# Kernel optimization log

Hardware: AMD Instinct MI355X
Metric: run time of the kernel (lower is better)

The kernel has to match this reference:

```python
import jax, jax.numpy as jnp
import numpy as np

B, S, D, H, DK, FF, NQ = 4, 1024, 512, 64, 8, 2048, 8


def _layernorm(x, w, b, eps=1e-5):
    m = x.mean(-1, keepdims=True)
    v = ((x - m) ** 2).mean(-1, keepdims=True)
    return (x - m) / jnp.sqrt(v + eps) * w + b


def setup_inputs() -> dict:
    key = jax.random.key(0)
    ks = jax.random.split(key, 24)
    std = 0.02
    inp = {
        "x": jax.random.normal(ks[0], (B, S, D), dtype=jnp.float32),
        "Wq": jax.random.normal(ks[1], (D, D)) * std,
        "bq": jnp.zeros((D,)),
        "Wk": jax.random.normal(ks[2], (D, D)) * std,
        "bk": jnp.zeros((D,)),
        "Wv": jax.random.normal(ks[3], (D, D)) * std,
        "bv": jnp.zeros((D,)),
        "theta_attn": jax.random.normal(ks[4], (DK,)) * 0.1,  # trainable RX angles
        "gate_attn": jnp.asarray(1.0, dtype=jnp.float32),
        "Wo": jax.random.normal(ks[5], (D, D)) * std,
        "bo": jnp.zeros((D,)),
        "ln1_w": jnp.ones((D,)),
        "ln1_b": jnp.zeros((D,)),
        "W1": jax.random.normal(ks[6], (FF, NQ)) * std,
        "b1": jnp.zeros((FF,)),
        "W2": jax.random.normal(ks[7], (D, FF)) * std,
        "b2": jnp.zeros((D,)),
        "phi_ffn": jax.random.normal(ks[8], (NQ,)) * 0.1,  # trainable RY angles
        "gate_ffn": jnp.asarray(1.0, dtype=jnp.float32),
        "ln2_w": jnp.ones((D,)),
        "ln2_b": jnp.zeros((D,)),
    }
    return inp


def _attention(x, Wq, bq, Wk, bk, Wv, bv, theta, gate, Wo, bo):
    q = x @ Wq.T + bq
    k = x @ Wk.T + bk
    v = x @ Wv.T + bv
    sep = lambda t: t.reshape(B, S, H, DK).transpose(0, 2, 1, 3)  # [B,H,S,DK]
    qh, kh, vh = sep(q), sep(k), sep(v)
    scores = jnp.einsum("bhsd,bhtd->bhst", qh, kh) / np.sqrt(DK)
    probs = jax.nn.softmax(scores, axis=-1)
    classical = jnp.einsum("bhst,bhtd->bhsd", probs, vh)
    classical = classical.transpose(0, 2, 1, 3).reshape(B, S, D)
    # Quantum head: RX(x_i) then RX(theta_i) -> RX(x_i+theta_i), CNOT ring, <Z_j>.
    # Analytic expectations: <Z_0> = prod_{k=1..DK-1} cos(a_k);
    #                        <Z_j> = prod_{k=0..j}    cos(a_k)   (j >= 1).
    cos_a = jnp.cos(qh + theta)  # [B,H,S,DK]
    cp = jnp.cumprod(cos_a, axis=-1)
    z0 = jnp.prod(cos_a[..., 1:], axis=-1, keepdims=True)
    quantum = jnp.concatenate([z0, cp[..., 1:]], axis=-1)  # [B,H,S,DK]
    quantum = quantum.transpose(0, 2, 1, 3).reshape(B, S, D)
    out = gate * quantum + (1.0 - gate) * classical
    return out @ Wo.T + bo


def _ffn(x, W1, b1, W2, b2, phi, gate):
    xs = x[..., :NQ]  # encoder uses first NQ features
    # Quantum: RX(x_i) then RY(phi_i), measure <Z_i> = cos(x_i)*cos(phi_i).
    qm = jnp.cos(xs) * jnp.cos(phi)
    quantum = jax.nn.relu(qm @ W1.T + b1) @ W2.T + b2
    classical = jax.nn.relu(xs @ W1.T + b1) @ W2.T + b2
    return gate * quantum + (1.0 - gate) * classical


def reference(x, Wq, bq, Wk, bk, Wv, bv, theta_attn, gate_attn, Wo, bo,
              ln1_w, ln1_b, W1, b1, W2, b2, phi_ffn, gate_ffn, ln2_w, ln2_b):
    attn_out = _attention(x, Wq, bq, Wk, bk, Wv, bv, theta_attn, gate_attn, Wo, bo)
    x1 = _layernorm(x + attn_out, ln1_w, ln1_b)
    ffn_out = _ffn(x1, W1, b1, W2, b2, phi_ffn, gate_ffn)
    return _layernorm(x1 + ffn_out, ln2_w, ln2_b)
```

## Files before the change

kernel.cpp:

```cpp
#include <hip/hip_runtime.h>
#include <hip/hip_bf16.h>


typedef short short8 __attribute__((ext_vector_type(8)));
typedef float floatx4 __attribute__((ext_vector_type(4)));

__device__ __forceinline__ unsigned short f2bf_bits(float f) {
  __hip_bfloat16 h = __float2bfloat16(f);
  return *reinterpret_cast<unsigned short*>(&h);
}
__device__ __forceinline__ float bfbits2f(unsigned short u) {
  union { unsigned int u; float f; } c;
  c.u = (unsigned int)u << 16;
  return c.f;
}

#define GLOBAL_LOAD_LDS16(g, l)                                               \
  __builtin_amdgcn_global_load_lds(                                           \
      (const __attribute__((address_space(1))) void*)(g),                     \
      (__attribute__((address_space(3))) void*)(l), 16, 0, 0)

#define WAIT_VMCNT0()   asm volatile("s_waitcnt vmcnt(0)" ::: "memory")
#define WAIT_VMCNT8()   asm volatile("s_waitcnt vmcnt(8)" ::: "memory")
#define WAIT_VMCNT10()  asm volatile("s_waitcnt vmcnt(10)" ::: "memory")
#define WAIT_VMCNT16()  asm volatile("s_waitcnt vmcnt(16)" ::: "memory")
#define WAIT_LGKM0()    asm volatile("s_waitcnt lgkmcnt(0)" ::: "memory")
#define BARRIER()       __builtin_amdgcn_s_barrier()
#define CFENCE()        asm volatile("" ::: "memory")

__device__ __forceinline__ void gemm_core_ks(
    const __hip_bfloat16* __restrict__ A,
    const __hip_bfloat16* __restrict__ W,
    int K, int kbeg, int ntiles, long m0, long n0, int lane,
    __hip_bfloat16* sh, floatx4 acc[4][4])
{
  const int srow = lane >> 3;
  const int gchunk = (lane & 7) ^ srow;
  const int frow = lane & 15;
  const int fk = lane >> 4;

  auto stage = [&](int kt, __hip_bfloat16* buf) {
#pragma unroll
    for (int ib = 0; ib < 8; ++ib) {
      const int row = ib * 8 + srow;
      GLOBAL_LOAD_LDS16(A + (m0 + row) * K + kt + gchunk * 8, buf + ib * 512);
      GLOBAL_LOAD_LDS16(W + (n0 + row) * K + kt + gchunk * 8, buf + 4096 + ib * 512);
    }
  };

  WAIT_LGKM0();
  stage(kbeg, sh);
  if (ntiles > 1) stage(kbeg + 64, sh + 8192);

  for (int t = 0; t < ntiles; ++t) {
    __hip_bfloat16* buf = sh + (t & 1) * 8192;
    if (t < ntiles - 1) { WAIT_VMCNT16(); }
    else               { WAIT_VMCNT0(); }

    short8 af[2][4], bf[2][4];
#pragma unroll
    for (int ks = 0; ks < 2; ++ks)
#pragma unroll
      for (int i = 0; i < 4; ++i) {
        const int ar = i * 16 + frow;
        af[ks][i] = *(const short8*)(buf + ar * 64 + (((ks * 4 + fk) ^ (ar & 7)) << 3));
        bf[ks][i] = *(const short8*)(buf + 4096 + ar * 64 + (((ks * 4 + fk) ^ (ar & 7)) << 3));
      }
    WAIT_LGKM0();
    if (t + 2 < ntiles) stage(kbeg + ((t + 2) << 6), buf);
#pragma unroll
    for (int ks = 0; ks < 2; ++ks)
#pragma unroll
      for (int i = 0; i < 4; ++i)
#pragma unroll
        for (int j = 0; j < 4; ++j)
          acc[i][j] = __builtin_amdgcn_mfma_f32_16x16x32_bf16(
              af[ks][i], bf[ks][j], acc[i][j], 0, 0, 0);
  }
}

__device__ __forceinline__ bool ks_reduce(
    floatx4 acc[4][4], __hip_bfloat16* sh, int wid, int lane)
{
  float* red = (float*)(sh + 16384);
  if (wid == 1) {
#pragma unroll
    for (int i = 0; i < 4; ++i)
#pragma unroll
      for (int j = 0; j < 4; ++j)
        *(floatx4*)(red + ((i * 4 + j) * 64 + lane) * 4) = acc[i][j];
    WAIT_LGKM0();
  }
  CFENCE(); BARRIER(); CFENCE();
  if (wid == 1) return false;
#pragma unroll
  for (int i = 0; i < 4; ++i)
#pragma unroll
    for (int j = 0; j < 4; ++j)
      acc[i][j] += *(const floatx4*)(red + ((i * 4 + j) * 64 + lane) * 4);
  return true;
}

__device__ __forceinline__ void store_f32(
    floatx4 acc[4][4], float* __restrict__ C, const float* __restrict__ bias,
    long m0, long n0, int lane)
{
  const int col_l = lane & 15;
  const int row_l = (lane >> 4) << 2;
#pragma unroll
  for (int j = 0; j < 4; ++j) {
    const long col = n0 + j * 16 + col_l;
    const float bv = bias[col];
#pragma unroll
    for (int i = 0; i < 4; ++i)
#pragma unroll
      for (int r = 0; r < 4; ++r)
        C[(m0 + i * 16 + row_l + r) * 512 + col] = acc[i][j][r] + bv;
  }
}

__device__ __forceinline__ void store_bf16(
    floatx4 acc[4][4], __hip_bfloat16* __restrict__ C,
    const float* __restrict__ bias, long m0, long n0, int lane)
{
  const int col_l = lane & 15;
  const int row_l = (lane >> 4) << 2;
#pragma unroll
  for (int j = 0; j < 4; ++j) {
    const long col = n0 + j * 16 + col_l;
    const float bv = bias[col];
#pragma unroll
    for (int i = 0; i < 4; ++i)
#pragma unroll
      for (int r = 0; r < 4; ++r)
        C[(m0 + i * 16 + row_l + r) * 512 + col] =
            __float2bfloat16(acc[i][j][r] + bv);
  }
}

__global__ __launch_bounds__(128) void gemm_qkv(
    const __hip_bfloat16* __restrict__ x_bf,
    const __hip_bfloat16* __restrict__ Wq,
    const __hip_bfloat16* __restrict__ Wk,
    const __hip_bfloat16* __restrict__ Wv,
    const float* __restrict__ bq, const float* __restrict__ bk,
    const float* __restrict__ bvv,
    __hip_bfloat16* __restrict__ mix,
    float* __restrict__ Qb, float* __restrict__ Kb, float* __restrict__ Vb,
    const float* __restrict__ theta, const float* __restrict__ gateA)
{
  const int z = blockIdx.z;
  const float g = *gateA;
  if (z > 0 && g == 1.0f) return;
  const __hip_bfloat16* W = (z == 0) ? Wq : (z == 1) ? Wk : Wv;
  const float* bias = (z == 0) ? bq : (z == 1) ? bk : bvv;
  float* Cf = (z == 0) ? Qb : (z == 1) ? Kb : Vb;

  __shared__ __align__(16) __hip_bfloat16 sh[32768];
  const int tid = threadIdx.x;
  const int wid = tid >> 6;
  const int lane = tid & 63;
  const long m0 = (long)blockIdx.x * 64;
  const long n0 = (long)blockIdx.y * 64;
  floatx4 acc[4][4];
#pragma unroll
  for (int i = 0; i < 4; ++i)
#pragma unroll
    for (int j = 0; j < 4; ++j) acc[i][j] = (floatx4){0.f, 0.f, 0.f, 0.f};

  gemm_core_ks(x_bf, W, 512, wid * 256, 4, m0, n0, lane, sh + wid * 16384, acc);
  if (!ks_reduce(acc, sh, wid, lane)) return;

  const int col_l = lane & 15;
  const int row_l = (lane >> 4) << 2;

  if (z > 0 || g != 1.0f) store_f32(acc, Cf, bias, m0, n0, lane);
  if (z == 0) {
    float* shf = (float*)sh;
    WAIT_LGKM0();
#pragma unroll
    for (int j = 0; j < 4; ++j) {
      const long col = n0 + j * 16 + col_l;
      const float bv = bias[col];
#pragma unroll
      for (int i = 0; i < 4; ++i)
#pragma unroll
        for (int r = 0; r < 4; ++r)
          shf[(i * 16 + row_l + r) * 64 + j * 16 + col_l] = acc[i][j][r] + bv;
    }
    WAIT_LGKM0();
    float th[8];
#pragma unroll
    for (int i = 0; i < 8; ++i) th[i] = theta[i];
#pragma unroll
    for (int t = 0; t < 8; ++t) {
      const int gidx = t * 64 + lane;
      const int row = gidx >> 3;
      const int hh = gidx & 7;
      const float* src = shf + row * 64 + hh * 8;
      float c[8];
#pragma unroll
      for (int i = 0; i < 8; ++i) c[i] = __cosf(src[i] + th[i]);
      float o[8];
      float p = c[1];
#pragma unroll
      for (int i = 2; i < 8; ++i) p *= c[i];
      o[0] = p;
      float cp = c[0];
#pragma unroll
      for (int i = 1; i < 8; ++i) { cp *= c[i]; o[i] = cp; }
      union { unsigned short u16[8]; uint4 v; } pk;
#pragma unroll
      for (int i = 0; i < 8; ++i) pk.u16[i] = f2bf_bits(o[i]);
      *(uint4*)(mix + (m0 + row) * 512 + n0 + hh * 8) = pk.v;
    }
  }
}

__global__ __launch_bounds__(512) void wo_lnffn(
    const __hip_bfloat16* __restrict__ A,
    const __hip_bfloat16* __restrict__ W,
    const float* __restrict__ bo,
    const float* __restrict__ x,
    const float* __restrict__ lw, const float* __restrict__ lb,
    float* __restrict__ x1, const float* __restrict__ phi,
    const float* __restrict__ W1,
    const float* __restrict__ b1,
    __hip_bfloat16* __restrict__ hq, __hip_bfloat16* __restrict__ hc,
    const float* __restrict__ gateF)
{
  __shared__ __align__(16) __hip_bfloat16 sh[68608];
  const int tid = threadIdx.x;
  const int wid = tid >> 6;
  const int lane = tid & 63;
  const long m0 = (long)blockIdx.x * 16;
  const long n0w = (long)wid * 64;

  const int srow = lane >> 3;
  const int gchunk = (lane & 7) ^ srow;
  const int frow = lane & 15;
  const int fk = lane >> 4;

  __hip_bfloat16* shA = sh;
  __hip_bfloat16* shW = sh + 3072 + wid * 8192;

  auto stageA = [&](int kt, int slot) {
    __hip_bfloat16* buf = shA + slot * 1024;
#pragma unroll
    for (int i = 0; i < 2; ++i) {
      const int row = i * 8 + srow;
      GLOBAL_LOAD_LDS16(A + (m0 + row) * 512 + kt + gchunk * 8, buf + i * 512);
    }
  };
  auto stageW = [&](int kt, int slot) {
    __hip_bfloat16* buf = shW + slot * 4096;
#pragma unroll
    for (int i = 0; i < 8; ++i) {
      const int row = i * 8 + srow;
      GLOBAL_LOAD_LDS16(W + (n0w + row) * 512 + kt + gchunk * 8, buf + i * 512);
    }
  };

  floatx4 acc[4];
#pragma unroll
  for (int j = 0; j < 4; ++j) acc[j] = (floatx4){0.f, 0.f, 0.f, 0.f};

  if (wid == 0) stageA(0, 0);
  stageW(0, 0);
  if (wid == 0) stageA(64, 1);
  stageW(64, 1);

  for (int t = 0; t < 8; ++t) {
    const int wslot = t & 1;
    const int aslot = t % 3;
    if (t < 7) { if (wid == 0) WAIT_VMCNT10(); else WAIT_VMCNT8(); }
    else       { WAIT_VMCNT0(); }
    BARRIER();

    short8 af[2], bf[2][4];
#pragma unroll
    for (int ks = 0; ks < 2; ++ks) {
      af[ks] = *(const short8*)(shA + aslot * 1024 + frow * 64 +
                                (((ks * 4 + fk) ^ (frow & 7)) << 3));
#pragma unroll
      for (int j = 0; j < 4; ++j) {
        const int wr = j * 16 + frow;
        bf[ks][j] = *(const short8*)(shW + wslot * 4096 + wr * 64 +
                                     (((ks * 4 + fk) ^ (frow & 7)) << 3));
      }
    }
    WAIT_LGKM0();
    if (t < 6) {
      if (wid == 0) stageA((t + 2) << 6, (t + 2) % 3);
      stageW((t + 2) << 6, wslot);
    }
#pragma unroll
    for (int ks = 0; ks < 2; ++ks)
#pragma unroll
      for (int j = 0; j < 4; ++j)
        acc[j] = __builtin_amdgcn_mfma_f32_16x16x32_bf16(
            af[ks], bf[ks][j], acc[j], 0, 0, 0);
  }

  BARRIER();

  float* attnL = (float*)sh;
  float* qmL = attnL + 16 * 516;
  float* xsL = qmL + 128;
  {
    const int col_l = lane & 15;
    const int row_l = (lane >> 4) << 2;
#pragma unroll
    for (int j = 0; j < 4; ++j) {
      const int c = (int)n0w + j * 16 + col_l;
      const float bv = bo[c];
#pragma unroll
      for (int r = 0; r < 4; ++r)
        attnL[(row_l + r) * 516 + c] = acc[j][r] + bv;
    }
  }
  WAIT_LGKM0();
  BARRIER();

  const int rr = tid >> 5;
  const int cl = tid & 31;
  const long rowg = m0 + rr;
  float sv[16];
  float sum = 0.f, ssq = 0.f;
#pragma unroll
  for (int i = 0; i < 16; ++i) {
    const int c = cl + i * 32;
    const float v = x[rowg * 512 + c] + attnL[rr * 516 + c];
    sv[i] = v; sum += v; ssq += v * v;
  }
#pragma unroll
  for (int off = 16; off > 0; off >>= 1) {
    sum += __shfl_xor(sum, off, 32);
    ssq += __shfl_xor(ssq, off, 32);
  }
  const float mean = sum * (1.0f / 512.0f);
  const float var = ssq * (1.0f / 512.0f) - mean * mean;
  const float rstd = rsqrtf(fmaxf(var, 0.0f) + 1e-5f);
#pragma unroll
  for (int i = 0; i < 16; ++i) {
    const int c = cl + i * 32;
    const float o = (sv[i] - mean) * rstd * lw[c] + lb[c];
    x1[rowg * 512 + c] = o;
    if (i == 0 && cl < 8) {
      qmL[rr * 8 + cl] = __cosf(o) * __cosf(phi[cl]);
      xsL[rr * 8 + cl] = o;
    }
  }
  WAIT_LGKM0();
  BARRIER();

  const int n4 = tid << 2;
  float w1r[4][8];
#pragma unroll
  for (int jr = 0; jr < 4; ++jr) {
    float4 wa = *(const float4*)(W1 + (long)(n4 + jr) * 8);
    float4 wb = *(const float4*)(W1 + (long)(n4 + jr) * 8 + 4);
    w1r[jr][0] = wa.x; w1r[jr][1] = wa.y; w1r[jr][2] = wa.z; w1r[jr][3] = wa.w;
    w1r[jr][4] = wb.x; w1r[jr][5] = wb.y; w1r[jr][6] = wb.z; w1r[jr][7] = wb.w;
  }
  float4 bb = *(const float4*)(b1 + n4);
  const float b1a[4] = {bb.x, bb.y, bb.z, bb.w};
  const float gv = *gateF;
#pragma unroll 2
  for (int r = 0; r < 16; ++r) {
    float qm8[8];
#pragma unroll
    for (int k = 0; k < 8; ++k) qm8[k] = qmL[r * 8 + k];
    union { unsigned short u16[4]; ushort4 v; } pk;
#pragma unroll
    for (int jr = 0; jr < 4; ++jr) {
      float a = b1a[jr];
#pragma unroll
      for (int k = 0; k < 8; ++k) a += qm8[k] * w1r[jr][k];
      pk.u16[jr] = f2bf_bits(fmaxf(a, 0.0f));
    }
    *(ushort4*)(hq + (m0 + r) * 2048 + n4) = pk.v;
    if (gv != 1.0f) {
      float xs8[8];
#pragma unroll
      for (int k = 0; k < 8; ++k) xs8[k] = xsL[r * 8 + k];
#pragma unroll
      for (int jr = 0; jr < 4; ++jr) {
        float a = b1a[jr];
#pragma unroll
        for (int k = 0; k < 8; ++k) a += xs8[k] * w1r[jr][k];
        pk.u16[jr] = f2bf_bits(fmaxf(a, 0.0f));
      }
      *(ushort4*)(hc + (m0 + r) * 2048 + n4) = pk.v;
    }
  }
}

__global__ __launch_bounds__(128) void gemm_ffnout(
    const __hip_bfloat16* __restrict__ hq,
    const __hip_bfloat16* __restrict__ hc,
    const __hip_bfloat16* __restrict__ W2, const float* __restrict__ b2,
    __hip_bfloat16* __restrict__ Fb, __hip_bfloat16* __restrict__ Fc,
    const float* __restrict__ gateF)
{
  const int z = blockIdx.z;
  if (z == 1 && *gateF == 1.0f) return;
  const __hip_bfloat16* A = z ? hc : hq;
  __hip_bfloat16* C = z ? Fc : Fb;
  __shared__ __align__(16) __hip_bfloat16 sh[32768];
  const int tid = threadIdx.x;
  const int wid = tid >> 6;
  const int lane = tid & 63;
  const long m0 = (long)blockIdx.x * 64;
  const long n0 = (long)blockIdx.y * 64;
  floatx4 acc[4][4];
#pragma unroll
  for (int i = 0; i < 4; ++i)
#pragma unroll
    for (int j = 0; j < 4; ++j) acc[i][j] = (floatx4){0.f, 0.f, 0.f, 0.f};
  gemm_core_ks(A, W2, 2048, wid * 1024, 16, m0, n0, lane, sh + wid * 16384, acc);
  if (!ks_reduce(acc, sh, wid, lane)) return;
  store_bf16(acc, C, b2, m0, n0, lane);
}

__device__ __forceinline__ void cvt_one(const float* s, __hip_bfloat16* d, int n,
                                        long tid, long stride) {
  const int n4 = n >> 2;
  for (long i = tid; i < n4; i += stride) {
    float4 v = ((const float4*)s)[i];
    ushort4 u;
    u.x = f2bf_bits(v.x); u.y = f2bf_bits(v.y);
    u.z = f2bf_bits(v.z); u.w = f2bf_bits(v.w);
    ((ushort4*)d)[i] = u;
  }
}

__global__ __launch_bounds__(256) void prep_inputs(
    const float* x, __hip_bfloat16* x_bf,
    const float* Wq, __hip_bfloat16* Wq_bf,
    const float* Wo, __hip_bfloat16* Wo_bf,
    const float* W2, __hip_bfloat16* W2_bf,
    const float* Wk, __hip_bfloat16* Wk_bf,
    const float* Wv, __hip_bfloat16* Wv_bf,
    const float* gateA)
{
  const long stride = (long)gridDim.x * blockDim.x;
  const long tid = (long)blockIdx.x * blockDim.x + threadIdx.x;
  cvt_one(x, x_bf, 4096 * 512, tid, stride);
  cvt_one(Wq, Wq_bf, 512 * 512, tid, stride);
  cvt_one(Wo, Wo_bf, 512 * 512, tid, stride);
  cvt_one(W2, W2_bf, 512 * 2048, tid, stride);
  if (*gateA != 1.0f) {
    cvt_one(Wk, Wk_bf, 512 * 512, tid, stride);
    cvt_one(Wv, Wv_bf, 512 * 512, tid, stride);
  }
}

__global__ __launch_bounds__(256) void attn_blend(
    const float* __restrict__ Qb, const float* __restrict__ Kb,
    const float* __restrict__ Vb, __hip_bfloat16* __restrict__ mix,
    const float* __restrict__ gateA)
{
  const float g = *gateA;
  if (g == 1.0f) return;
  const int idx = blockIdx.x * blockDim.x + threadIdx.x;
  if (idx >= 4 * 64 * 1024) return;
  const int s = idx & 1023;
  const int h = (idx >> 10) & 63;
  const int b = idx >> 16;
  const long qoff = ((long)(b * 1024 + s)) * 512 + h * 8;
  float q[8];
#pragma unroll
  for (int i = 0; i < 8; ++i) q[i] = Qb[qoff + i] * 0.35355339059327373f;
  float m = -INFINITY, l = 0.0f, acc[8];
#pragma unroll
  for (int i = 0; i < 8; ++i) acc[i] = 0.0f;
  for (int t = 0; t < 1024; ++t) {
    const long koff = ((long)(b * 1024 + t)) * 512 + h * 8;
    const float* kr = Kb + koff;
    const float* vr = Vb + koff;
    float sc = 0.0f;
#pragma unroll
    for (int i = 0; i < 8; ++i) sc += q[i] * kr[i];
    float nm = fmaxf(m, sc);
    float corr = __expf(m - nm);
    float p = __expf(sc - nm);
    l = l * corr + p;
#pragma unroll
    for (int i = 0; i < 8; ++i) acc[i] = acc[i] * corr + p * vr[i];
    m = nm;
  }
  const float inv = 1.0f / l;
  union { unsigned short u16[8]; uint4 v; } pk;
  pk.v = *(const uint4*)(mix + qoff);
#pragma unroll
  for (int i = 0; i < 8; ++i) {
    float quant = bfbits2f(pk.u16[i]);
    pk.u16[i] = f2bf_bits(g * quant + (1.0f - g) * acc[i] * inv);
  }
  *(uint4*)(mix + qoff) = pk.v;
}

__global__ __launch_bounds__(256) void add_ln3(
    const float* __restrict__ x1, const __hip_bfloat16* __restrict__ Fb,
    const __hip_bfloat16* __restrict__ Fc, const float* __restrict__ gateF,
    const float* __restrict__ lw, const float* __restrict__ lb,
    float* __restrict__ out)
{
  const int tid = threadIdx.x;
  const int wv = tid >> 6, lane = tid & 63;
  const int row = blockIdx.x * 4 + wv;
  const long base = (long)row * 512;
  const int c0 = lane * 8;
  float4 a0 = *(const float4*)(x1 + base + c0);
  float4 a1 = *(const float4*)(x1 + base + c0 + 4);
  union { unsigned short u16[8]; uint4 v; } fb;
  fb.v = *(const uint4*)(Fb + base + c0);
  const float xa[8] = {a0.x, a0.y, a0.z, a0.w, a1.x, a1.y, a1.z, a1.w};
  float s[8];
  const float gv = *gateF;
  if (gv != 1.0f) {
    union { unsigned short u16[8]; uint4 v; } fc;
    fc.v = *(const uint4*)(Fc + base + c0);
    const float om = 1.0f - gv;
#pragma unroll
    for (int i = 0; i < 8; ++i)
      s[i] = xa[i] + gv * bfbits2f(fb.u16[i]) + om * bfbits2f(fc.u16[i]);
  } else {
#pragma unroll
    for (int i = 0; i < 8; ++i) s[i] = xa[i] + bfbits2f(fb.u16[i]);
  }
  float sum = 0.f, ssq = 0.f;
#pragma unroll
  for (int i = 0; i < 8; ++i) { sum += s[i]; ssq += s[i] * s[i]; }
#pragma unroll
  for (int off = 32; off > 0; off >>= 1) {
    sum += __shfl_xor(sum, off);
    ssq += __shfl_xor(ssq, off);
  }
  const float mean = sum * (1.0f / 512.0f);
  const float var = ssq * (1.0f / 512.0f) - mean * mean;
  const float rstd = rsqrtf(fmaxf(var, 0.0f) + 1e-5f);
  float4 w0 = *(const float4*)(lw + c0);
  float4 w1 = *(const float4*)(lw + c0 + 4);
  float4 g0 = *(const float4*)(lb + c0);
  float4 g1 = *(const float4*)(lb + c0 + 4);
  const float wf[8] = {w0.x, w0.y, w0.z, w0.w, w1.x, w1.y, w1.z, w1.w};
  const float gf8[8] = {g0.x, g0.y, g0.z, g0.w, g1.x, g1.y, g1.z, g1.w};
  float o[8];
#pragma unroll
  for (int i = 0; i < 8; ++i) o[i] = (s[i] - mean) * rstd * wf[i] + gf8[i];
  *(float4*)(out + base + c0) = (float4){o[0], o[1], o[2], o[3]};
  *(float4*)(out + base + c0 + 4) = (float4){o[4], o[5], o[6], o[7]};
}

extern "C" void kernel_launch(void* const* d_in, const int* in_sizes, int n_in,
                              void* d_out, int out_size, void* d_ws, size_t ws_size,
                              hipStream_t stream) {
  const float* x     = (const float*)d_in[0];
  const float* Wq    = (const float*)d_in[1];
  const float* bq    = (const float*)d_in[2];
  const float* Wk    = (const float*)d_in[3];
  const float* bk    = (const float*)d_in[4];
  const float* Wv    = (const float*)d_in[5];
  const float* bv    = (const float*)d_in[6];
  const float* theta = (const float*)d_in[7];
  const float* gateA = (const float*)d_in[8];
  const float* Wo    = (const float*)d_in[9];
  const float* bo    = (const float*)d_in[10];
  const float* ln1w  = (const float*)d_in[11];
  const float* ln1b  = (const float*)d_in[12];
  const float* W1    = (const float*)d_in[13];
  const float* b1    = (const float*)d_in[14];
  const float* W2    = (const float*)d_in[15];
  const float* b2    = (const float*)d_in[16];
  const float* phi   = (const float*)d_in[17];
  const float* gateF = (const float*)d_in[18];
  const float* ln2w  = (const float*)d_in[19];
  const float* ln2b  = (const float*)d_in[20];
  float* out = (float*)d_out;

  const size_t MB = 1024 * 1024;
  char* wsb = (char*)d_ws;
  __hip_bfloat16* x_bf    = (__hip_bfloat16*)(wsb + 0 * MB);
  __hip_bfloat16* Wq_bf   = (__hip_bfloat16*)(wsb + 4 * MB);
  __hip_bfloat16* Wo_bf   = (__hip_bfloat16*)(wsb + 4 * MB + 512 * 1024);
  __hip_bfloat16* W2_bf   = (__hip_bfloat16*)(wsb + 5 * MB);
  __hip_bfloat16* mix_bf  = (__hip_bfloat16*)(wsb + 8 * MB);
  float*          x1      = (float*)(wsb + 16 * MB);
  __hip_bfloat16* hq_bf   = (__hip_bfloat16*)(wsb + 24 * MB);
  __hip_bfloat16* Fb_bf   = (__hip_bfloat16*)(wsb + 40 * MB);
  float*          Qb      = (float*)(wsb + 52 * MB);
  __hip_bfloat16* Wk_bf   = (__hip_bfloat16*)(wsb + 60 * MB);
  __hip_bfloat16* Wv_bf   = (__hip_bfloat16*)(wsb + 60 * MB + 512 * 1024);
  float*          Kb2     = (float*)(wsb + 61 * MB);
  float*          Vb2     = (float*)(wsb + 69 * MB);
  __hip_bfloat16* hc_bf   = (__hip_bfloat16*)(wsb + 77 * MB);
  __hip_bfloat16* Fc_bf   = (__hip_bfloat16*)(wsb + 93 * MB);

  prep_inputs<<<1024, 256, 0, stream>>>(
      x, x_bf, Wq, Wq_bf, Wo, Wo_bf, W2, W2_bf, Wk, Wk_bf, Wv, Wv_bf, gateA);
  gemm_qkv<<<dim3(64, 8, 3), 128, 0, stream>>>(
      x_bf, Wq_bf, Wk_bf, Wv_bf, bq, bk, bv,
      mix_bf, Qb, Kb2, Vb2, theta, gateA);
  attn_blend<<<1024, 256, 0, stream>>>(Qb, Kb2, Vb2, mix_bf, gateA);
  wo_lnffn<<<256, 512, 0, stream>>>(
      mix_bf, Wo_bf, bo, x, ln1w, ln1b, x1, phi, W1, b1, hq_bf, hc_bf, gateF);
  gemm_ffnout<<<dim3(64, 8, 2), 128, 0, stream>>>(
      hq_bf, hc_bf, W2_bf, b2, Fb_bf, Fc_bf, gateF);
  add_ln3<<<1024, 256, 0, stream>>>(x1, Fb_bf, Fc_bf, gateF, ln2w, ln2b, out);
}
```

Baseline: 146.3 us.

## Load GEMM fragments directly from global and split K across four waves

Replaces the LDS-staged, double-buffered GEMM core in the QKV and FFN-out kernels with direct global-to-register fragment loads and a register ping-pong. The K dimension is split across four waves instead of two, and the partials are reduced through shared memory. This drops LDS staging traffic and raises per-block parallelism, at the cost of uncoalesced 16-byte global loads and a larger reduction. It also changes the swizzle index in the wo_lnffn W-fragment load from frow to wr.

```diff
diff --git a/kernel.cpp b/kernel.cpp
--- a/kernel.cpp
+++ b/kernel.cpp
@@ -4,6 +4,8 @@
 
 typedef short short8 __attribute__((ext_vector_type(8)));
 typedef float floatx4 __attribute__((ext_vector_type(4)));
+
+#define MFMA_BF16 __builtin_amdgcn_mfma_f32_16x16x32_bf16
 
 __device__ __forceinline__ unsigned short f2bf_bits(float f) {
   __hip_bfloat16 h = __float2bfloat16(f);
@@ -23,81 +25,85 @@
 #define WAIT_VMCNT0()   asm volatile("s_waitcnt vmcnt(0)" ::: "memory")
 #define WAIT_VMCNT8()   asm volatile("s_waitcnt vmcnt(8)" ::: "memory")
 #define WAIT_VMCNT10()  asm volatile("s_waitcnt vmcnt(10)" ::: "memory")
-#define WAIT_VMCNT16()  asm volatile("s_waitcnt vmcnt(16)" ::: "memory")
 #define WAIT_LGKM0()    asm volatile("s_waitcnt lgkmcnt(0)" ::: "memory")
 #define BARRIER()       __builtin_amdgcn_s_barrier()
 #define CFENCE()        asm volatile("" ::: "memory")
 
-__device__ __forceinline__ void gemm_core_ks(
+__device__ __forceinline__ void frag_load(
+    short8 af[2][4], short8 bf[2][4],
+    const __hip_bfloat16* const pa[4], const __hip_bfloat16* const pw[4],
+    int koff)
+{
+#pragma unroll
+  for (int i = 0; i < 4; ++i) {
+    af[0][i] = *(const short8*)(pa[i] + koff);
+    af[1][i] = *(const short8*)(pa[i] + koff + 32);
+    bf[0][i] = *(const short8*)(pw[i] + koff);
+    bf[1][i] = *(const short8*)(pw[i] + koff + 32);
+  }
+}
+
+__device__ __forceinline__ void mfma_step(
+    short8 af[2][4], short8 bf[2][4], floatx4 acc[4][4])
+{
+#pragma unroll
+  for (int ks = 0; ks < 2; ++ks)
+#pragma unroll
+    for (int i = 0; i < 4; ++i)
+#pragma unroll
+      for (int j = 0; j < 4; ++j)
+        acc[i][j] = MFMA_BF16(af[ks][i], bf[ks][j], acc[i][j], 0, 0, 0);
+}
+
+template<int NSTEP>
+__device__ __forceinline__ void gemm_direct(
     const __hip_bfloat16* __restrict__ A,
     const __hip_bfloat16* __restrict__ W,
-    int K, int kbeg, int ntiles, long m0, long n0, int lane,
-    __hip_bfloat16* sh, floatx4 acc[4][4])
-{
-  const int srow = lane >> 3;
-  const int gchunk = (lane & 7) ^ srow;
+    int K, int kbeg, long m0, long n0, int lane,
+    floatx4 acc[4][4])
+{
   const int frow = lane & 15;
   const int fk = lane >> 4;
-
-  auto stage = [&](int kt, __hip_bfloat16* buf) {
-#pragma unroll
-    for (int ib = 0; ib < 8; ++ib) {
-      const int row = ib * 8 + srow;
-      GLOBAL_LOAD_LDS16(A + (m0 + row) * K + kt + gchunk * 8, buf + ib * 512);
-      GLOBAL_LOAD_LDS16(W + (n0 + row) * K + kt + gchunk * 8, buf + 4096 + ib * 512);
-    }
-  };
-
-  WAIT_LGKM0();
-  stage(kbeg, sh);
-  if (ntiles > 1) stage(kbeg + 64, sh + 8192);
-
-  for (int t = 0; t < ntiles; ++t) {
-    __hip_bfloat16* buf = sh + (t & 1) * 8192;
-    if (t < ntiles - 1) { WAIT_VMCNT16(); }
-    else               { WAIT_VMCNT0(); }
-
-    short8 af[2][4], bf[2][4];
-#pragma unroll
-    for (int ks = 0; ks < 2; ++ks)
-#pragma unroll
-      for (int i = 0; i < 4; ++i) {
-        const int ar = i * 16 + frow;
-        af[ks][i] = *(const short8*)(buf + ar * 64 + (((ks * 4 + fk) ^ (ar & 7)) << 3));
-        bf[ks][i] = *(const short8*)(buf + 4096 + ar * 64 + (((ks * 4 + fk) ^ (ar & 7)) << 3));
-      }
+  const __hip_bfloat16* pa[4];
+  const __hip_bfloat16* pw[4];
+#pragma unroll
+  for (int i = 0; i < 4; ++i) {
+    pa[i] = A + (m0 + i * 16 + frow) * (long)K + kbeg + fk * 8;
+    pw[i] = W + (n0 + i * 16 + frow) * (long)K + kbeg + fk * 8;
+  }
+  short8 aA[2][4], bA[2][4], aB[2][4], bB[2][4];
+  frag_load(aA, bA, pa, pw, 0);
+#pragma unroll 1
+  for (int tt = 0; tt < NSTEP / 2; ++tt) {
+    frag_load(aB, bB, pa, pw, tt * 128 + 64);
+    mfma_step(aA, bA, acc);
+    if (tt + 1 < NSTEP / 2) frag_load(aA, bA, pa, pw, tt * 128 + 128);
+    mfma_step(aB, bB, acc);
+  }
+}
+
+__device__ __forceinline__ bool ks_reduce4(
+    floatx4 acc[4][4], float* red, int wid, int lane)
+{
+  if (wid > 0) {
+    float* my = red + (wid - 1) * 4096;
+#pragma unroll
+    for (int i = 0; i < 4; ++i)
+#pragma unroll
+      for (int j = 0; j < 4; ++j)
+        *(floatx4*)(my + ((i * 4 + j) * 64 + lane) * 4) = acc[i][j];
     WAIT_LGKM0();
-    if (t + 2 < ntiles) stage(kbeg + ((t + 2) << 6), buf);
-#pragma unroll
-    for (int ks = 0; ks < 2; ++ks)
-#pragma unroll
-      for (int i = 0; i < 4; ++i)
-#pragma unroll
-        for (int j = 0; j < 4; ++j)
-          acc[i][j] = __builtin_amdgcn_mfma_f32_16x16x32_bf16(
-              af[ks][i], bf[ks][j], acc[i][j], 0, 0, 0);
-  }
-}
-
-__device__ __forceinline__ bool ks_reduce(
-    floatx4 acc[4][4], __hip_bfloat16* sh, int wid, int lane)
-{
-  float* red = (float*)(sh + 16384);
-  if (wid == 1) {
+  }
+  CFENCE(); BARRIER(); CFENCE();
+  if (wid > 0) return false;
+#pragma unroll
+  for (int w = 0; w < 3; ++w)
 #pragma unroll
     for (int i = 0; i < 4; ++i)
 #pragma unroll
       for (int j = 0; j < 4; ++j)
-        *(floatx4*)(red + ((i * 4 + j) * 64 + lane) * 4) = acc[i][j];
-    WAIT_LGKM0();
-  }
-  CFENCE(); BARRIER(); CFENCE();
-  if (wid == 1) return false;
-#pragma unroll
-  for (int i = 0; i < 4; ++i)
-#pragma unroll
-    for (int j = 0; j < 4; ++j)
-      acc[i][j] += *(const floatx4*)(red + ((i * 4 + j) * 64 + lane) * 4);
+        acc[i][j] += *(const floatx4*)(red + w * 4096 +
+                                       ((i * 4 + j) * 64 + lane) * 4);
   return true;
 }
 
@@ -138,7 +144,7 @@
   }
 }
 
-__global__ __launch_bounds__(128) void gemm_qkv(
+__global__ __launch_bounds__(256, 2) void gemm_qkv(
     const __hip_bfloat16* __restrict__ x_bf,
     const __hip_bfloat16* __restrict__ Wq,
     const __hip_bfloat16* __restrict__ Wk,
@@ -156,7 +162,7 @@
   const float* bias = (z == 0) ? bq : (z == 1) ? bk : bvv;
   float* Cf = (z == 0) ? Qb : (z == 1) ? Kb : Vb;
 
-  __shared__ __align__(16) __hip_bfloat16 sh[32768];
+  __shared__ __align__(16) float shred[12288];
   const int tid = threadIdx.x;
   const int wid = tid >> 6;
   const int lane = tid & 63;
@@ -168,15 +174,15 @@
 #pragma unroll
     for (int j = 0; j < 4; ++j) acc[i][j] = (floatx4){0.f, 0.f, 0.f, 0.f};
 
-  gemm_core_ks(x_bf, W, 512, wid * 256, 4, m0, n0, lane, sh + wid * 16384, acc);
-  if (!ks_reduce(acc, sh, wid, lane)) return;
+  gemm_direct<2>(x_bf, W, 512, wid * 128, m0, n0, lane, acc);
+  if (!ks_reduce4(acc, shred, wid, lane)) return;
 
   const int col_l = lane & 15;
   const int row_l = (lane >> 4) << 2;
 
   if (z > 0 || g != 1.0f) store_f32(acc, Cf, bias, m0, n0, lane);
   if (z == 0) {
-    float* shf = (float*)sh;
+    float* shf = shred;
     WAIT_LGKM0();
 #pragma unroll
     for (int j = 0; j < 4; ++j) {
@@ -286,7 +292,7 @@
       for (int j = 0; j < 4; ++j) {
         const int wr = j * 16 + frow;
         bf[ks][j] = *(const short8*)(shW + wslot * 4096 + wr * 64 +
-                                     (((ks * 4 + fk) ^ (frow & 7)) << 3));
+                                     (((ks * 4 + fk) ^ (wr & 7)) << 3));
       }
     }
     WAIT_LGKM0();
@@ -396,7 +402,7 @@
   }
 }
 
-__global__ __launch_bounds__(128) void gemm_ffnout(
+__global__ __launch_bounds__(256, 2) void gemm_ffnout(
     const __hip_bfloat16* __restrict__ hq,
     const __hip_bfloat16* __restrict__ hc,
     const __hip_bfloat16* __restrict__ W2, const float* __restrict__ b2,
@@ -407,7 +413,7 @@
   if (z == 1 && *gateF == 1.0f) return;
   const __hip_bfloat16* A = z ? hc : hq;
   __hip_bfloat16* C = z ? Fc : Fb;
-  __shared__ __align__(16) __hip_bfloat16 sh[32768];
+  __shared__ __align__(16) float shred[12288];
   const int tid = threadIdx.x;
   const int wid = tid >> 6;
   const int lane = tid & 63;
@@ -418,8 +424,8 @@
   for (int i = 0; i < 4; ++i)
 #pragma unroll
     for (int j = 0; j < 4; ++j) acc[i][j] = (floatx4){0.f, 0.f, 0.f, 0.f};
-  gemm_core_ks(A, W2, 2048, wid * 1024, 16, m0, n0, lane, sh + wid * 16384, acc);
-  if (!ks_reduce(acc, sh, wid, lane)) return;
+  gemm_direct<8>(A, W2, 2048, wid * 512, m0, n0, lane, acc);
+  if (!ks_reduce4(acc, shred, wid, lane)) return;
   store_bf16(acc, C, b2, m0, n0, lane);
 }
 
@@ -600,13 +606,13 @@
 
   prep_inputs<<<1024, 256, 0, stream>>>(
       x, x_bf, Wq, Wq_bf, Wo, Wo_bf, W2, W2_bf, Wk, Wk_bf, Wv, Wv_bf, gateA);
-  gemm_qkv<<<dim3(64, 8, 3), 128, 0, stream>>>(
+  gemm_qkv<<<dim3(64, 8, 3), 256, 0, stream>>>(
       x_bf, Wq_bf, Wk_bf, Wv_bf, bq, bk, bv,
       mix_bf, Qb, Kb2, Vb2, theta, gateA);
   attn_blend<<<1024, 256, 0, stream>>>(Qb, Kb2, Vb2, mix_bf, gateA);
   wo_lnffn<<<256, 512, 0, stream>>>(
       mix_bf, Wo_bf, bo, x, ln1w, ln1b, x1, phi, W1, b1, hq_bf, hc_bf, gateF);
-  gemm_ffnout<<<dim3(64, 8, 2), 128, 0, stream>>>(
+  gemm_ffnout<<<dim3(64, 8, 2), 256, 0, stream>>>(
       hq_bf, hc_bf, W2_bf, b2, Fb_bf, Fc_bf, gateF);
   add_ln3<<<1024, 256, 0, stream>>>(x1, Fb_bf, Fc_bf, gateF, ln2w, ln2b, out);
 }
```

Result: slower. 167.9 us (+14.7%).

## Restructure FFN output GEMM into 16-row blocks with 8 waves spanning full N

Applied to the files above, without the earlier changes.

The FFN second GEMM drops its split-K 64x64 tiling with a cross-wave reduction. Each 512-thread block now owns 16 rows and all 512 output columns, with each wave taking a 64-column slice over the full K=2048. The A tile is staged once per block and shared by all waves through a 3-slot LDS ring, and W2 tiles are double-buffered per wave, which removes the split-K reduction and its LDS traffic. The W swizzle read index in the QKV kernel is also changed to use the row within the tile. The cost is a much larger LDS footprint per block, which lowers occupancy, and a longer serial K loop per wave.

```diff
diff --git a/kernel.cpp b/kernel.cpp
--- a/kernel.cpp
+++ b/kernel.cpp
@@ -116,25 +116,6 @@
 #pragma unroll
       for (int r = 0; r < 4; ++r)
         C[(m0 + i * 16 + row_l + r) * 512 + col] = acc[i][j][r] + bv;
-  }
-}
-
-__device__ __forceinline__ void store_bf16(
-    floatx4 acc[4][4], __hip_bfloat16* __restrict__ C,
-    const float* __restrict__ bias, long m0, long n0, int lane)
-{
-  const int col_l = lane & 15;
-  const int row_l = (lane >> 4) << 2;
-#pragma unroll
-  for (int j = 0; j < 4; ++j) {
-    const long col = n0 + j * 16 + col_l;
-    const float bv = bias[col];
-#pragma unroll
-    for (int i = 0; i < 4; ++i)
-#pragma unroll
-      for (int r = 0; r < 4; ++r)
-        C[(m0 + i * 16 + row_l + r) * 512 + col] =
-            __float2bfloat16(acc[i][j][r] + bv);
   }
 }
 
@@ -286,7 +267,7 @@
       for (int j = 0; j < 4; ++j) {
         const int wr = j * 16 + frow;
         bf[ks][j] = *(const short8*)(shW + wslot * 4096 + wr * 64 +
-                                     (((ks * 4 + fk) ^ (frow & 7)) << 3));
+                                     (((ks * 4 + fk) ^ (wr & 7)) << 3));
       }
     }
     WAIT_LGKM0();
@@ -396,31 +377,101 @@
   }
 }
 
-__global__ __launch_bounds__(128) void gemm_ffnout(
+__global__ __launch_bounds__(512) void gemm_ffnout(
     const __hip_bfloat16* __restrict__ hq,
     const __hip_bfloat16* __restrict__ hc,
     const __hip_bfloat16* __restrict__ W2, const float* __restrict__ b2,
     __hip_bfloat16* __restrict__ Fb, __hip_bfloat16* __restrict__ Fc,
     const float* __restrict__ gateF)
 {
-  const int z = blockIdx.z;
+  const int z = blockIdx.y;
   if (z == 1 && *gateF == 1.0f) return;
   const __hip_bfloat16* A = z ? hc : hq;
   __hip_bfloat16* C = z ? Fc : Fb;
-  __shared__ __align__(16) __hip_bfloat16 sh[32768];
+
+  __shared__ __align__(16) __hip_bfloat16 sh[68608];
   const int tid = threadIdx.x;
   const int wid = tid >> 6;
   const int lane = tid & 63;
-  const long m0 = (long)blockIdx.x * 64;
-  const long n0 = (long)blockIdx.y * 64;
-  floatx4 acc[4][4];
-#pragma unroll
-  for (int i = 0; i < 4; ++i)
-#pragma unroll
-    for (int j = 0; j < 4; ++j) acc[i][j] = (floatx4){0.f, 0.f, 0.f, 0.f};
-  gemm_core_ks(A, W2, 2048, wid * 1024, 16, m0, n0, lane, sh + wid * 16384, acc);
-  if (!ks_reduce(acc, sh, wid, lane)) return;
-  store_bf16(acc, C, b2, m0, n0, lane);
+  const long m0 = (long)blockIdx.x * 16;
+  const long n0w = (long)wid * 64;
+
+  const int srow = lane >> 3;
+  const int gchunk = (lane & 7) ^ srow;
+  const int frow = lane & 15;
+  const int fk = lane >> 4;
+
+  __hip_bfloat16* shA = sh;
+  __hip_bfloat16* shW = sh + 3072 + wid * 8192;
+
+  auto stageA = [&](int kt, int slot) {
+    __hip_bfloat16* buf = shA + slot * 1024;
+#pragma unroll
+    for (int i = 0; i < 2; ++i) {
+      const int row = i * 8 + srow;
+      GLOBAL_LOAD_LDS16(A + (m0 + row) * 2048 + kt + gchunk * 8, buf + i * 512);
+    }
+  };
+  auto stageW = [&](int kt, int slot) {
+    __hip_bfloat16* buf = shW + slot * 4096;
+#pragma unroll
+    for (int i = 0; i < 8; ++i) {
+      const int row = i * 8 + srow;
+      GLOBAL_LOAD_LDS16(W2 + (n0w + row) * 2048 + kt + gchunk * 8, buf + i * 512);
+    }
+  };
+
+  floatx4 acc[4];
+#pragma unroll
+  for (int j = 0; j < 4; ++j) acc[j] = (floatx4){0.f, 0.f, 0.f, 0.f};
+
+  if (wid == 0) stageA(0, 0);
+  stageW(0, 0);
+  if (wid == 0) stageA(64, 1);
+  stageW(64, 1);
+
+  for (int t = 0; t < 32; ++t) {
+    const int wslot = t & 1;
+    const int aslot = t % 3;
+    if (t < 31) { if (wid == 0) WAIT_VMCNT10(); else WAIT_VMCNT8(); }
+    else        { WAIT_VMCNT0(); }
+    BARRIER();
+
+    short8 af[2], bf[2][4];
+#pragma unroll
+    for (int ks = 0; ks < 2; ++ks) {
+      af[ks] = *(const short8*)(shA + aslot * 1024 + frow * 64 +
+                                (((ks * 4 + fk) ^ (frow & 7)) << 3));
+#pragma unroll
+      for (int j = 0; j < 4; ++j) {
+        const int wr = j * 16 + frow;
+        bf[ks][j] = *(const short8*)(shW + wslot * 4096 + wr * 64 +
+                                     (((ks * 4 + fk) ^ (wr & 7)) << 3));
+      }
+    }
+    WAIT_LGKM0();
+    if (t < 30) {
+      if (wid == 0) stageA((t + 2) << 6, (t + 2) % 3);
+      stageW((t + 2) << 6, wslot);
+    }
+#pragma unroll
+    for (int ks = 0; ks < 2; ++ks)
+#pragma unroll
+      for (int j = 0; j < 4; ++j)
+        acc[j] = __builtin_amdgcn_mfma_f32_16x16x32_bf16(
+            af[ks], bf[ks][j], acc[j], 0, 0, 0);
+  }
+
+  const int col_l = lane & 15;
+  const int row_l = (lane >> 4) << 2;
+#pragma unroll
+  for (int j = 0; j < 4; ++j) {
+    const long col = n0w + j * 16 + col_l;
+    const float bv = b2[col];
+#pragma unroll
+    for (int r = 0; r < 4; ++r)
+      C[(m0 + row_l + r) * 512 + col] = __float2bfloat16(acc[j][r] + bv);
+  }
 }
 
 __device__ __forceinline__ void cvt_one(const float* s, __hip_bfloat16* d, int n,
@@ -606,7 +657,7 @@
   attn_blend<<<1024, 256, 0, stream>>>(Qb, Kb2, Vb2, mix_bf, gateA);
   wo_lnffn<<<256, 512, 0, stream>>>(
       mix_bf, Wo_bf, bo, x, ln1w, ln1b, x1, phi, W1, b1, hq_bf, hc_bf, gateF);
-  gemm_ffnout<<<dim3(64, 8, 2), 128, 0, stream>>>(
+  gemm_ffnout<<<dim3(256, 2), 512, 0, stream>>>(
       hq_bf, hc_bf, W2_bf, b2, Fb_bf, Fc_bf, gateF);
   add_ln3<<<1024, 256, 0, stream>>>(x1, Fb_bf, Fc_bf, gateF, ln2w, ln2b, out);
 }
```

Measured after the change: 158.0 us. 1.08x slower.

## Replace split-K two-wave GEMM with cooperative N-split and shared 3-stage LDS

Applied to the files above, without the earlier changes.

The QKV and FFN-output GEMMs no longer split K across two waves with a final LDS reduction. Both waves now share one A/W tile: one wave stages A and the other stages W into a three-slot LDS ring guarded by barriers, and each wave computes half of the N columns. This removes the duplicated global loads and the cross-wave accumulator reduction, and cuts LDS usage, at the cost of per-tile barriers and fewer MFMAs per wave. It also fixes the swizzle index in the W fragment read of another kernel, using wr instead of frow.

```diff
diff --git a/kernel.cpp b/kernel.cpp
--- a/kernel.cpp
+++ b/kernel.cpp
@@ -23,93 +23,85 @@
 #define WAIT_VMCNT0()   asm volatile("s_waitcnt vmcnt(0)" ::: "memory")
 #define WAIT_VMCNT8()   asm volatile("s_waitcnt vmcnt(8)" ::: "memory")
 #define WAIT_VMCNT10()  asm volatile("s_waitcnt vmcnt(10)" ::: "memory")
-#define WAIT_VMCNT16()  asm volatile("s_waitcnt vmcnt(16)" ::: "memory")
 #define WAIT_LGKM0()    asm volatile("s_waitcnt lgkmcnt(0)" ::: "memory")
 #define BARRIER()       __builtin_amdgcn_s_barrier()
 #define CFENCE()        asm volatile("" ::: "memory")
 
-__device__ __forceinline__ void gemm_core_ks(
+template<int NT>
+__device__ __forceinline__ void gemm_coop2(
     const __hip_bfloat16* __restrict__ A,
     const __hip_bfloat16* __restrict__ W,
-    int K, int kbeg, int ntiles, long m0, long n0, int lane,
-    __hip_bfloat16* sh, floatx4 acc[4][4])
+    int K, long m0, long n0, int wid, int lane,
+    __hip_bfloat16* sh, floatx4 acc[4][2])
 {
   const int srow = lane >> 3;
   const int gchunk = (lane & 7) ^ srow;
   const int frow = lane & 15;
   const int fk = lane >> 4;
 
-  auto stage = [&](int kt, __hip_bfloat16* buf) {
+  const __hip_bfloat16* src = wid ? W : A;
+  const long r0 = wid ? n0 : m0;
+  const int dstoff = wid ? 4096 : 0;
+
+  auto stage = [&](int kt, int slot) {
+    __hip_bfloat16* buf = sh + slot * 8192 + dstoff;
 #pragma unroll
     for (int ib = 0; ib < 8; ++ib) {
       const int row = ib * 8 + srow;
-      GLOBAL_LOAD_LDS16(A + (m0 + row) * K + kt + gchunk * 8, buf + ib * 512);
-      GLOBAL_LOAD_LDS16(W + (n0 + row) * K + kt + gchunk * 8, buf + 4096 + ib * 512);
+      GLOBAL_LOAD_LDS16(src + (r0 + row) * (long)K + kt + gchunk * 8,
+                        buf + ib * 512);
     }
   };
 
   WAIT_LGKM0();
-  stage(kbeg, sh);
-  if (ntiles > 1) stage(kbeg + 64, sh + 8192);
-
-  for (int t = 0; t < ntiles; ++t) {
-    __hip_bfloat16* buf = sh + (t & 1) * 8192;
-    if (t < ntiles - 1) { WAIT_VMCNT16(); }
-    else               { WAIT_VMCNT0(); }
-
-    short8 af[2][4], bf[2][4];
-#pragma unroll
-    for (int ks = 0; ks < 2; ++ks)
+  stage(0, 0);
+  stage(64, 1);
+
+  for (int t = 0; t < NT; ++t) {
+    const int slot = t % 3;
+    if (t + 1 < NT) { WAIT_VMCNT8(); }
+    else            { WAIT_VMCNT0(); }
+    BARRIER();
+
+    __hip_bfloat16* buf = sh + slot * 8192;
+    short8 af[2][4], bf[2][2];
+#pragma unroll
+    for (int ks = 0; ks < 2; ++ks) {
 #pragma unroll
       for (int i = 0; i < 4; ++i) {
         const int ar = i * 16 + frow;
-        af[ks][i] = *(const short8*)(buf + ar * 64 + (((ks * 4 + fk) ^ (ar & 7)) << 3));
-        bf[ks][i] = *(const short8*)(buf + 4096 + ar * 64 + (((ks * 4 + fk) ^ (ar & 7)) << 3));
+        af[ks][i] = *(const short8*)(buf + ar * 64 +
+                                     (((ks * 4 + fk) ^ (ar & 7)) << 3));
       }
+#pragma unroll
+      for (int j = 0; j < 2; ++j) {
+        const int wr = wid * 32 + j * 16 + frow;
+        bf[ks][j] = *(const short8*)(buf + 4096 + wr * 64 +
+                                     (((ks * 4 + fk) ^ (wr & 7)) << 3));
+      }
+    }
     WAIT_LGKM0();
-    if (t + 2 < ntiles) stage(kbeg + ((t + 2) << 6), buf);
+    if (t + 2 < NT) stage((t + 2) << 6, (t + 2) % 3);
 #pragma unroll
     for (int ks = 0; ks < 2; ++ks)
 #pragma unroll
       for (int i = 0; i < 4; ++i)
 #pragma unroll
-        for (int j = 0; j < 4; ++j)
+        for (int j = 0; j < 2; ++j)
           acc[i][j] = __builtin_amdgcn_mfma_f32_16x16x32_bf16(
               af[ks][i], bf[ks][j], acc[i][j], 0, 0, 0);
   }
 }
 
-__device__ __forceinline__ bool ks_reduce(
-    floatx4 acc[4][4], __hip_bfloat16* sh, int wid, int lane)
-{
-  float* red = (float*)(sh + 16384);
-  if (wid == 1) {
-#pragma unroll
-    for (int i = 0; i < 4; ++i)
-#pragma unroll
-      for (int j = 0; j < 4; ++j)
-        *(floatx4*)(red + ((i * 4 + j) * 64 + lane) * 4) = acc[i][j];
-    WAIT_LGKM0();
-  }
-  CFENCE(); BARRIER(); CFENCE();
-  if (wid == 1) return false;
-#pragma unroll
-  for (int i = 0; i < 4; ++i)
-#pragma unroll
-    for (int j = 0; j < 4; ++j)
-      acc[i][j] += *(const floatx4*)(red + ((i * 4 + j) * 64 + lane) * 4);
-  return true;
-}
-
-__device__ __forceinline__ void store_f32(
-    floatx4 acc[4][4], float* __restrict__ C, const float* __restrict__ bias,
-    long m0, long n0, int lane)
+__device__ __forceinline__ void store_f32_half(
+    floatx4 acc[4][2], float* __restrict__ C, const float* __restrict__ bias,
+    long m0, long n0h, int lane)
 {
   const int col_l = lane & 15;
   const int row_l = (lane >> 4) << 2;
 #pragma unroll
-  for (int j = 0; j < 4; ++j) {
-    const long col = n0 + j * 16 + col_l;
+  for (int j = 0; j < 2; ++j) {
+    const long col = n0h + j * 16 + col_l;
     const float bv = bias[col];
 #pragma unroll
     for (int i = 0; i < 4; ++i)
@@ -119,15 +111,15 @@
   }
 }
 
-__device__ __forceinline__ void store_bf16(
-    floatx4 acc[4][4], __hip_bfloat16* __restrict__ C,
-    const float* __restrict__ bias, long m0, long n0, int lane)
+__device__ __forceinline__ void store_bf16_half(
+    floatx4 acc[4][2], __hip_bfloat16* __restrict__ C,
+    const float* __restrict__ bias, long m0, long n0h, int lane)
 {
   const int col_l = lane & 15;
   const int row_l = (lane >> 4) << 2;
 #pragma unroll
-  for (int j = 0; j < 4; ++j) {
-    const long col = n0 + j * 16 + col_l;
+  for (int j = 0; j < 2; ++j) {
+    const long col = n0h + j * 16 + col_l;
     const float bv = bias[col];
 #pragma unroll
     for (int i = 0; i < 4; ++i)
@@ -156,45 +148,47 @@
   const float* bias = (z == 0) ? bq : (z == 1) ? bk : bvv;
   float* Cf = (z == 0) ? Qb : (z == 1) ? Kb : Vb;
 
-  __shared__ __align__(16) __hip_bfloat16 sh[32768];
+  __shared__ __align__(16) __hip_bfloat16 sh[24576];
   const int tid = threadIdx.x;
   const int wid = tid >> 6;
   const int lane = tid & 63;
   const long m0 = (long)blockIdx.x * 64;
   const long n0 = (long)blockIdx.y * 64;
-  floatx4 acc[4][4];
+  floatx4 acc[4][2];
 #pragma unroll
   for (int i = 0; i < 4; ++i)
 #pragma unroll
-    for (int j = 0; j < 4; ++j) acc[i][j] = (floatx4){0.f, 0.f, 0.f, 0.f};
-
-  gemm_core_ks(x_bf, W, 512, wid * 256, 4, m0, n0, lane, sh + wid * 16384, acc);
-  if (!ks_reduce(acc, sh, wid, lane)) return;
-
-  const int col_l = lane & 15;
-  const int row_l = (lane >> 4) << 2;
-
-  if (z > 0 || g != 1.0f) store_f32(acc, Cf, bias, m0, n0, lane);
+    for (int j = 0; j < 2; ++j) acc[i][j] = (floatx4){0.f, 0.f, 0.f, 0.f};
+
+  gemm_coop2<8>(x_bf, W, 512, m0, n0, wid, lane, sh, acc);
+
+  if (z > 0 || g != 1.0f)
+    store_f32_half(acc, Cf, bias, m0, n0 + wid * 32, lane);
+
   if (z == 0) {
     float* shf = (float*)sh;
+    const int col_l = lane & 15;
+    const int row_l = (lane >> 4) << 2;
     WAIT_LGKM0();
-#pragma unroll
-    for (int j = 0; j < 4; ++j) {
-      const long col = n0 + j * 16 + col_l;
-      const float bv = bias[col];
+    CFENCE(); BARRIER(); CFENCE();
+#pragma unroll
+    for (int j = 0; j < 2; ++j) {
+      const int c = wid * 32 + j * 16 + col_l;
+      const float bv = bias[n0 + c];
 #pragma unroll
       for (int i = 0; i < 4; ++i)
 #pragma unroll
         for (int r = 0; r < 4; ++r)
-          shf[(i * 16 + row_l + r) * 64 + j * 16 + col_l] = acc[i][j][r] + bv;
+          shf[(i * 16 + row_l + r) * 64 + c] = acc[i][j][r] + bv;
     }
     WAIT_LGKM0();
+    CFENCE(); BARRIER(); CFENCE();
     float th[8];
 #pragma unroll
     for (int i = 0; i < 8; ++i) th[i] = theta[i];
 #pragma unroll
-    for (int t = 0; t < 8; ++t) {
-      const int gidx = t * 64 + lane;
+    for (int q = 0; q < 4; ++q) {
+      const int gidx = (wid * 4 + q) * 64 + lane;
       const int row = gidx >> 3;
       const int hh = gidx & 7;
       const float* src = shf + row * 64 + hh * 8;
@@ -286,7 +280,7 @@
       for (int j = 0; j < 4; ++j) {
         const int wr = j * 16 + frow;
         bf[ks][j] = *(const short8*)(shW + wslot * 4096 + wr * 64 +
-                                     (((ks * 4 + fk) ^ (frow & 7)) << 3));
+                                     (((ks * 4 + fk) ^ (wr & 7)) << 3));
       }
     }
     WAIT_LGKM0();
@@ -407,20 +401,19 @@
   if (z == 1 && *gateF == 1.0f) return;
   const __hip_bfloat16* A = z ? hc : hq;
   __hip_bfloat16* C = z ? Fc : Fb;
-  __shared__ __align__(16) __hip_bfloat16 sh[32768];
+  __shared__ __align__(16) __hip_bfloat16 sh[24576];
   const int tid = threadIdx.x;
   const int wid = tid >> 6;
   const int lane = tid & 63;
   const long m0 = (long)blockIdx.x * 64;
   const long n0 = (long)blockIdx.y * 64;
-  floatx4 acc[4][4];
+  floatx4 acc[4][2];
 #pragma unroll
   for (int i = 0; i < 4; ++i)
 #pragma unroll
-    for (int j = 0; j < 4; ++j) acc[i][j] = (floatx4){0.f, 0.f, 0.f, 0.f};
-  gemm_core_ks(A, W2, 2048, wid * 1024, 16, m0, n0, lane, sh + wid * 16384, acc);
-  if (!ks_reduce(acc, sh, wid, lane)) return;
-  store_bf16(acc, C, b2, m0, n0, lane);
+    for (int j = 0; j < 2; ++j) acc[i][j] = (floatx4){0.f, 0.f, 0.f, 0.f};
+  gemm_coop2<32>(A, W2, 2048, m0, n0, wid, lane, sh, acc);
+  store_bf16_half(acc, C, b2, m0, n0 + wid * 32, lane);
 }
 
 __device__ __forceinline__ void cvt_one(const float* s, __hip_bfloat16* d, int n,
```

Result: slower. 149.5 us (+2.2%).
